# Performance work log

Measured on AMD Instinct MI355X. Metric: run time of the kernel, lower is better.

Reference implementation:

```python
import jax, jax.numpy as jnp
import numpy as np

N_U, N_I, D_IN_U, D_IN_I, D, D_QOL, B = 4096, 4096, 256, 256, 256, 4, 8192

def _w(key, shape, scale=0.05):
    return (jax.random.normal(key, shape) * scale).astype(jnp.float32)

def setup_inputs() -> dict:
    key = jax.random.key(0)
    ks = jax.random.split(key, 24)
    inp = {
        "x_u": jax.random.normal(ks[0], (N_U, D_IN_U), jnp.float32),
        "x_i": jax.random.normal(ks[1], (N_I, D_IN_I), jnp.float32),
        "social_adj": jax.random.randint(ks[2], (N_U, N_U), 0, 2, jnp.int32),
        "ui_adj": jax.random.randint(ks[3], (N_U, N_I), 0, 2, jnp.int32),
        "user_idx": jax.random.randint(ks[4], (B,), 0, N_U, jnp.int32),
        "item_idx": jax.random.randint(ks[5], (B,), 0, N_I, jnp.int32),
        "q_u": jax.random.normal(ks[6], (N_U, D_QOL), jnp.float32),
        # params (Linear stored as [in, out]; y = x @ W + b)
        "user_W": _w(ks[7], (D_IN_U, D)), "user_b": jnp.zeros((D,), jnp.float32),
        "item_W": _w(ks[8], (D_IN_I, D)), "item_b": jnp.zeros((D,), jnp.float32),
        "soc_W": _w(ks[9], (D, D)), "soc_a": _w(ks[10], (2 * D,)),
        "cnt_W": _w(ks[11], (D, D)), "cnt_a": _w(ks[12], (2 * D,)),
        "gate_W": _w(ks[13], (D_QOL, D)), "gate_b": jnp.zeros((D,), jnp.float32),
        "qproj_W": _w(ks[14], (D_QOL, D)), "qproj_b": jnp.zeros((D,), jnp.float32),
        "alpha_q": jnp.float32(0.3),
        "pred_W1": _w(ks[15], (2 * D, D)), "pred_b1": jnp.zeros((D,), jnp.float32),
        "pred_W2": _w(ks[16], (D, 1)), "pred_b2": jnp.zeros((1,), jnp.float32),
    }
    return inp

def _gat(Wh_src, Wh_dst, a, adj):
    """GAT additive attention: src rows attend over dst cols where adj!=0.
    Rows with no neighbors produce zero output (matches nan_to_num + zeroing)."""
    d = Wh_src.shape[-1]
    a1 = Wh_src @ a[:d]          # [N_src]
    a2 = Wh_dst @ a[d:]          # [N_dst]
    e = jax.nn.leaky_relu(a1[:, None] + a2[None, :], 0.2)  # [N_src, N_dst]
    mask = adj != 0
    neg_inf = jnp.float32(-jnp.inf)
    m = jnp.max(jnp.where(mask, e, neg_inf), axis=-1, keepdims=True)
    m = jnp.where(jnp.isfinite(m), m, 0.0)  # guard empty rows
    ex = jnp.where(mask, jnp.exp(e - m), 0.0)
    denom = jnp.sum(ex, axis=-1, keepdims=True)
    alpha = jnp.where(denom > 0, ex / jnp.where(denom > 0, denom, 1.0), 0.0)
    out = alpha @ Wh_dst
    return out, alpha

def reference(x_u, x_i, social_adj, ui_adj, user_idx, item_idx, q_u,
              user_W, user_b, item_W, item_b, soc_W, soc_a, cnt_W, cnt_a,
              gate_W, gate_b, qproj_W, qproj_b, alpha_q,
              pred_W1, pred_b1, pred_W2, pred_b2):
    h_u = x_u @ user_W + user_b               # [N_u, D]
    h_i = x_i @ item_W + item_b               # [N_i, D]
    # social attention (users over users)
    Wh = h_u @ soc_W
    soc_msg, alpha_s = _gat(Wh, Wh, soc_a, social_adj)
    # content attention (users over items)
    Wu = h_u @ cnt_W
    Wi = h_i @ cnt_W
    cnt_msg, alpha_c = _gat(Wu, Wi, cnt_a, ui_adj)
    h_u_out = jax.nn.elu(soc_msg + cnt_msg + h_u)
    # QoL gate
    gate = jax.nn.sigmoid(q_u @ gate_W + gate_b)
    qproj = q_u @ qproj_W + qproj_b
    h_u_out = h_u_out + alpha_q * gate * qproj
    # pair prediction (dropout inactive at eval)
    cat = jnp.concatenate([h_u_out[user_idx], h_i[item_idx]], axis=-1)  # [B, 2D]
    hid = jax.nn.relu(cat @ pred_W1 + pred_b1)
    r = (hid @ pred_W2 + pred_b2)[..., 0]
    r_hat = 1.0 + 4.0 * jax.nn.sigmoid(r)
    return r_hat, alpha_s, alpha_c
```

## Files before the change

kernel.cpp:

```cpp
#include <hip/hip_runtime.h>

typedef unsigned short u16;
typedef unsigned int u32;
typedef unsigned char u8;
typedef unsigned long long u64;
typedef float f32x4 __attribute__((ext_vector_type(4)));
typedef __bf16 bf16x8 __attribute__((ext_vector_type(8)));

#define NU 4096
#define DD 256
#define BB 8192

__device__ inline u16 f2b(float f) {
    u32 u = __builtin_bit_cast(u32, f);
    u32 r = (u + 0x7fffu + ((u >> 16) & 1u)) >> 16;
    return (u16)r;
}
__device__ inline float b2f(u16 v) { return __builtin_bit_cast(float, (u32)v << 16); }
__device__ inline float lrelu(float x) { return x > 0.f ? x : 0.2f * x; }
__device__ inline float decmax(u32 e) {
    return __builtin_bit_cast(float, (e >> 31) ? (e & 0x7fffffffu) : ~e);
}

#define BARRIER_LGKM() asm volatile("s_waitcnt lgkmcnt(0)\ns_barrier" ::: "memory")

__global__ __launch_bounds__(256) void k_pro(
    const float* __restrict__ x_u, const float* __restrict__ x_i,
    const float* __restrict__ user_W, const float* __restrict__ item_W, const float* __restrict__ pred_W1,
    const float* __restrict__ soc_W, const float* __restrict__ soc_a,
    const float* __restrict__ cnt_W, const float* __restrict__ cnt_a,
    const float* __restrict__ user_b, const float* __restrict__ item_b,
    u16* __restrict__ xu_b, u16* __restrict__ xi_b,
    u16* __restrict__ uWt, u16* __restrict__ iWt, u16* __restrict__ p1Wt,
    float* __restrict__ uvec,
    u16* __restrict__ WusT, u16* __restrict__ WicT,
    float* __restrict__ b_us, float* __restrict__ b_ic, u32* __restrict__ MhEnc) {
    __shared__ float t[64][65];
    __shared__ float sa[256];
    const int b = blockIdx.x;
    const int tid = threadIdx.x;

    if (b < 1024) {
        const float* in = (b < 512) ? x_u : x_i;
        u16* out = (b < 512) ? xu_b : xi_b;
        int i = (b & 511) * 256 + tid;
        const float4 v0 = *(const float4*)(in + (size_t)i * 8);
        const float4 v1 = *(const float4*)(in + (size_t)i * 8 + 4);
        u16 u[8] = {f2b(v0.x), f2b(v0.y), f2b(v0.z), f2b(v0.w),
                    f2b(v1.x), f2b(v1.y), f2b(v1.z), f2b(v1.w)};
        *(uint4*)(out + (size_t)i * 8) = *(uint4*)u;
    } else if (b < 1088) {
        int j = b - 1024;
        const float* in;
        u16* out;
        int R;
        if (j < 16) { in = user_W; out = uWt; R = 256; }
        else if (j < 32) { in = item_W; out = iWt; R = 256; j -= 16; }
        else { in = pred_W1; out = p1Wt; R = 512; j -= 32; }
        int rb = (j >> 2) * 64, cb = (j & 3) * 64;
        for (int k = 0; k < 16; ++k) {
            int idx = k * 256 + tid;
            int lr = idx >> 6, lc = idx & 63;
            t[lr][lc] = in[(size_t)(rb + lr) * 256 + cb + lc];
        }
        __syncthreads();
        for (int k = 0; k < 16; ++k) {
            int idx = k * 256 + tid;
            int lr = idx >> 6, lc = idx & 63;
            out[(size_t)(cb + lr) * R + rb + lc] = f2b(t[lc][lr]);
        }
    } else if (b < 1092) {
        int bb = b - 1088;
        if (bb == 0 && tid < 2) MhEnc[tid] = 0u;
        const float* W = (bb < 2) ? soc_W : cnt_W;
        const float* a = ((bb < 2) ? soc_a : cnt_a) + (bb & 1) * 256;
        int lane = tid & 63, wv = tid >> 6;
        sa[tid] = a[tid];
        __syncthreads();
        for (int rr = 0; rr < 64; ++rr) {
            int in = wv * 64 + rr;
            float4 w4 = *(const float4*)(W + (size_t)in * 256 + lane * 4);
            float acc = w4.x * sa[lane * 4] + w4.y * sa[lane * 4 + 1] + w4.z * sa[lane * 4 + 2] + w4.w * sa[lane * 4 + 3];
#pragma unroll
            for (int off = 32; off; off >>= 1) acc += __shfl_down(acc, off);
            if (lane == 0) uvec[bb * 256 + in] = acc;
        }
    } else {
        int j = b - 1092;
        int p = j >> 4;
        int tile = j & 15;
        const float* A = p ? item_W : user_W;
        const float* Bw = p ? cnt_W : soc_W;
        const float* bvec = p ? item_b : user_b;
        u16* outT = p ? WicT : WusT;
        float* outb = p ? b_ic : b_us;
        int m0 = (tile >> 2) * 64, n0 = (tile & 3) * 64;
        int m = m0 + (tid >> 4) * 4, n = n0 + (tid & 15) * 4;
        float acc[4][4];
#pragma unroll
        for (int i = 0; i < 4; ++i)
#pragma unroll
            for (int k = 0; k < 4; ++k) acc[i][k] = 0.f;
        for (int k0 = 0; k0 < 256; k0 += 4) {
            float aa[4][4], bb2[4][4];
#pragma unroll
            for (int i = 0; i < 4; ++i) {
                float4 v = *(const float4*)(A + (size_t)(m + i) * 256 + k0);
                aa[i][0] = v.x; aa[i][1] = v.y; aa[i][2] = v.z; aa[i][3] = v.w;
            }
#pragma unroll
            for (int k = 0; k < 4; ++k) {
                float4 v = *(const float4*)(Bw + (size_t)(k0 + k) * 256 + n);
                bb2[k][0] = v.x; bb2[k][1] = v.y; bb2[k][2] = v.z; bb2[k][3] = v.w;
            }
#pragma unroll
            for (int i = 0; i < 4; ++i)
#pragma unroll
                for (int k = 0; k < 4; ++k)
#pragma unroll
                    for (int jj = 0; jj < 4; ++jj) acc[i][jj] += aa[i][k] * bb2[k][jj];
        }
#pragma unroll
        for (int i = 0; i < 4; ++i)
#pragma unroll
            for (int jj = 0; jj < 4; ++jj) outT[(size_t)(n + jj) * 256 + m + i] = f2b(acc[i][jj]);
        if (tile >> 2 == 0 && tid < 64) {
            int nn = n0 + tid;
            float s = 0.f;
            for (int k = 0; k < 256; ++k) s += bvec[k] * Bw[(size_t)k * 256 + nn];
            outb[nn] = s;
        }
    }
}

__global__ __launch_bounds__(256) void k_gemm4(
    const u16* __restrict__ xu_b, const u16* __restrict__ xi_b,
    const u16* __restrict__ uWt, const u16* __restrict__ iWt,
    const u16* __restrict__ WusT, const u16* __restrict__ WicT,
    const float* __restrict__ user_b, const float* __restrict__ item_b,
    const float* __restrict__ b_us, const float* __restrict__ b_ic,
    float* __restrict__ h_u_f, float* __restrict__ h_i_f, u16* __restrict__ h_i_b,
    u16* __restrict__ WhT, u16* __restrict__ WiT) {
    const int z = blockIdx.z;
    const int M = 4096, N = 256, K = 256;
    const u16* A = (z == 0 || z == 2) ? xu_b : xi_b;
    const u16* Bt = (z == 0) ? uWt : (z == 1) ? iWt : (z == 2) ? WusT : WicT;
    const float* bias = (z == 0) ? user_b : (z == 1) ? item_b : (z == 2) ? b_us : b_ic;
    float* Cf = (z == 0) ? h_u_f : (z == 1) ? h_i_f : nullptr;
    u16* Cb = (z == 1) ? h_i_b : nullptr;
    u16* Cbt = (z == 2) ? WhT : (z == 3) ? WiT : nullptr;

    __shared__ u16 As[64 * 64];
    __shared__ u16 Bs[64 * 64];
    const int tid = threadIdx.x;
    const int lane = tid & 63, wv = tid >> 6;
    const int bm = blockIdx.x * 64, bn = blockIdx.y * 64;
    const int wm = (wv >> 1) * 32, wn = (wv & 1) * 32;
    f32x4 acc[2][2];
#pragma unroll
    for (int i = 0; i < 2; i++)
#pragma unroll
        for (int j = 0; j < 2; j++) acc[i][j] = f32x4{0.f, 0.f, 0.f, 0.f};

    char* Ab = (char*)As;
    char* Bb = (char*)Bs;
    const int r = tid >> 2;
    const int ib0 = (tid & 3) * 32;
    const int swz = (r & 7) << 4;

    for (int k0 = 0; k0 < K; k0 += 64) {
        const uint4* ga = (const uint4*)(A + (size_t)(bm + r) * K + k0 + (ib0 >> 1));
        const uint4* gb = (const uint4*)(Bt + (size_t)(bn + r) * K + k0 + (ib0 >> 1));
        uint4 va0 = ga[0], va1 = ga[1];
        uint4 vb0 = gb[0], vb1 = gb[1];
        __syncthreads();
        *(uint4*)(Ab + r * 128 + ((ib0) ^ swz)) = va0;
        *(uint4*)(Ab + r * 128 + ((ib0 + 16) ^ swz)) = va1;
        *(uint4*)(Bb + r * 128 + ((ib0) ^ swz)) = vb0;
        *(uint4*)(Bb + r * 128 + ((ib0 + 16) ^ swz)) = vb1;
        __syncthreads();
#pragma unroll
        for (int kh = 0; kh < 2; ++kh) {
            bf16x8 af[2], bfr[2];
#pragma unroll
            for (int mf = 0; mf < 2; ++mf) {
                int row = wm + mf * 16 + (lane & 15);
                int kb = kh * 64 + ((lane >> 4) << 4);
                af[mf] = *(const bf16x8*)(Ab + row * 128 + (kb ^ ((row & 7) << 4)));
            }
#pragma unroll
            for (int nf = 0; nf < 2; ++nf) {
                int row = wn + nf * 16 + (lane & 15);
                int kb = kh * 64 + ((lane >> 4) << 4);
                bfr[nf] = *(const bf16x8*)(Bb + row * 128 + (kb ^ ((row & 7) << 4)));
            }
#pragma unroll
            for (int mf = 0; mf < 2; ++mf)
#pragma unroll
                for (int nf = 0; nf < 2; ++nf)
                    acc[mf][nf] = __builtin_amdgcn_mfma_f32_16x16x32_bf16(af[mf], bfr[nf], acc[mf][nf], 0, 0, 0);
        }
    }
#pragma unroll
    for (int mf = 0; mf < 2; ++mf) {
#pragma unroll
        for (int nf = 0; nf < 2; ++nf) {
            int col = bn + wn + nf * 16 + (lane & 15);
            int row0 = bm + wm + mf * 16 + ((lane >> 4) << 2);
            float bv = bias[col];
            float v[4];
#pragma unroll
            for (int q = 0; q < 4; ++q) {
                float x = acc[mf][nf][q] + bv;
                v[q] = x;
                if (Cf) Cf[(size_t)(row0 + q) * N + col] = x;
                if (Cb) Cb[(size_t)(row0 + q) * N + col] = f2b(x);
            }
            if (Cbt) {
                uint2 p;
                p.x = (u32)f2b(v[0]) | ((u32)f2b(v[1]) << 16);
                p.y = (u32)f2b(v[2]) | ((u32)f2b(v[3]) << 16);
                *(uint2*)(Cbt + (size_t)col * M + row0) = p;
            }
        }
    }
}

__global__ __launch_bounds__(256) void k_gemv_a(const float* __restrict__ h_u, const float* __restrict__ h_i,
                                                const float* __restrict__ uvec, float* __restrict__ avec,
                                                u32* __restrict__ MhEnc) {
    int tid = threadIdx.x, lane = tid & 63, wv = tid >> 6;
    int ib = blockIdx.x * 64;
    const float* H = (wv == 3) ? h_i : h_u;
    const float* u = uvec + wv * 256;
    float4 u4 = *(const float4*)(u + lane * 4);
    float runm = -1e30f;
    for (int rr = 0; rr < 64; ++rr) {
        int row = ib + rr;
        float4 h4 = *(const float4*)(H + (size_t)row * 256 + lane * 4);
        float acc = h4.x * u4.x + h4.y * u4.y + h4.z * u4.z + h4.w * u4.w;
#pragma unroll
        for (int off = 32; off; off >>= 1) acc += __shfl_down(acc, off);
        if (lane == 0) {
            avec[wv * 4096 + row] = acc;
            runm = fmaxf(runm, acc);
        }
    }
    if (lane == 0 && (wv & 1)) {
        u32 b = __builtin_bit_cast(u32, runm);
        u32 e = (b >> 31) ? ~b : (b | 0x80000000u);
        atomicMax(&MhEnc[wv >> 1], e);
    }
}

__global__ __launch_bounds__(256) void k_scan(const int* __restrict__ adjS, const int* __restrict__ adjC,
                                              const float* __restrict__ avec, const u32* __restrict__ MhEnc,
                                              float* __restrict__ dpart, u8* __restrict__ bits) {
    int z = blockIdx.z;
    const int* adj = z ? adjC : adjS;
    const float* a1 = avec + z * 8192;
    const float* a2 = a1 + 4096;
    u8* bz = bits + (size_t)z * 2097152;
    float mhg = decmax(MhEnc[z]);
    int ib = blockIdx.x * 64, jb = blockIdx.y * 512;
    int lane = threadIdx.x & 63, wv = threadIdx.x >> 6;
    float4 A0 = *(const float4*)(a2 + jb + lane * 8);
    float4 A1 = *(const float4*)(a2 + jb + lane * 8 + 4);
    const int boff = blockIdx.y * 64 + (lane & 7) * 8 + (lane >> 3);
    for (int rr = 0; rr < 16; ++rr) {
        int row = ib + wv * 16 + rr;
        float a1r = a1[row];
        float mr = lrelu(a1r + mhg);
        const int4* p = (const int4*)(adj + (size_t)row * 4096 + jb + lane * 8);
        int4 v0 = p[0], v1 = p[1];
        u32 b = (u32)(v0.x != 0) | ((u32)(v0.y != 0) << 1) | ((u32)(v0.z != 0) << 2) | ((u32)(v0.w != 0) << 3) |
                ((u32)(v1.x != 0) << 4) | ((u32)(v1.y != 0) << 5) | ((u32)(v1.z != 0) << 6) | ((u32)(v1.w != 0) << 7);
        bz[(size_t)row * 512 + boff] = (u8)b;
        float acc = 0.f;
        acc += v0.x ? __expf(lrelu(a1r + A0.x) - mr) : 0.f;
        acc += v0.y ? __expf(lrelu(a1r + A0.y) - mr) : 0.f;
        acc += v0.z ? __expf(lrelu(a1r + A0.z) - mr) : 0.f;
        acc += v0.w ? __expf(lrelu(a1r + A0.w) - mr) : 0.f;
        acc += v1.x ? __expf(lrelu(a1r + A1.x) - mr) : 0.f;
        acc += v1.y ? __expf(lrelu(a1r + A1.y) - mr) : 0.f;
        acc += v1.z ? __expf(lrelu(a1r + A1.z) - mr) : 0.f;
        acc += v1.w ? __expf(lrelu(a1r + A1.w) - mr) : 0.f;
#pragma unroll
        for (int off = 32; off; off >>= 1) acc += __shfl_down(acc, off);
        if (lane == 0) dpart[((size_t)z * 8 + blockIdx.y) * 4096 + row] = acc;
    }
}

__global__ __launch_bounds__(512, 4) void k_flash(const u8* __restrict__ bits,
                                                  const float* __restrict__ avec, const u32* __restrict__ MhEnc,
                                                  const float* __restrict__ dpart,
                                                  const u16* __restrict__ WhT, const u16* __restrict__ WiT,
                                                  float* __restrict__ out, u16* __restrict__ msgpart) {
    const int z = blockIdx.z;
    const int ib = blockIdx.x * 64;
    const int jb = blockIdx.y * 512;
    const int tid = threadIdx.x, lane = tid & 63, wv = tid >> 6;
    const u8* bz = bits + (size_t)z * 2097152;
    const float* a1 = avec + z * 8192;
    const float* a2 = a1 + 4096;
    const u16* Pt = z ? WiT : WhT;
    float* alpha = out + 8192 + (size_t)z * 16777216;

    __shared__ float a2s[512];
    __shared__ u16 Atile[2 * 64 * 64];
    __shared__ float s_a1[64], s_mr[64], s_inv[64];
    char* Ab = (char*)Atile;

    a2s[tid] = a2[jb + tid];
    if (tid < 64) {
        float a = a1[ib + tid];
        float mhg = decmax(MhEnc[z]);
        s_a1[tid] = a;
        s_mr[tid] = lrelu(a + mhg);
        float d = 0.f;
#pragma unroll
        for (int s = 0; s < 8; ++s) d += dpart[((size_t)(z * 8 + s)) * 4096 + ib + tid];
        s_inv[tid] = d > 0.f ? 1.f / d : 0.f;
    }
    __syncthreads();

    const int row = wv * 8 + (lane >> 3);
    const int cg = lane & 7;
    const int gr = ib + row;
    const u64 b64 = *(const u64*)(bz + (size_t)gr * 512 + (jb >> 9) * 64 + cg * 8);
    const float a1r = s_a1[row], mr = s_mr[row], ivr = s_inv[row];
    const int wswz = (row & 7) << 4;

    const u16* ptb0 = Pt + (size_t)(wv * 32 + (lane & 15)) * 4096 + jb + ((lane >> 4) << 3);
    const u16* ptb1 = ptb0 + (size_t)16 * 4096;

    f32x4 acc[4][2];
#pragma unroll
    for (int i = 0; i < 4; i++)
#pragma unroll
        for (int j = 0; j < 2; j++) acc[i][j] = f32x4{0.f, 0.f, 0.f, 0.f};

    float al[8];
    auto compute_al = [&](int js, int buf) {
        const float4 a2a = *(const float4*)(a2s + js * 64 + cg * 8);
        const float4 a2b = *(const float4*)(a2s + js * 64 + cg * 8 + 4);
        u32 byte = (u32)(b64 >> (js * 8)) & 0xffu;
        float av[8] = {a2a.x, a2a.y, a2a.z, a2a.w, a2b.x, a2b.y, a2b.z, a2b.w};
#pragma unroll
        for (int k = 0; k < 8; ++k) {
            float e = lrelu(a1r + av[k]) - mr;
            al[k] = ((byte >> k) & 1) ? __expf(e) * ivr : 0.f;
        }
        u16 pk[8];
#pragma unroll
        for (int k = 0; k < 8; ++k) pk[k] = f2b(al[k]);
        *(uint4*)(Ab + buf * 8192 + row * 128 + ((cg * 16) ^ wswz)) = *(uint4*)pk;
    };

    compute_al(0, 0);
    BARRIER_LGKM();

    bf16x8 bcur[2][2], bnxt[2][2];
#pragma unroll
    for (int kh = 0; kh < 2; ++kh) {
        bcur[kh][0] = *(const bf16x8*)(ptb0 + kh * 32);
        bcur[kh][1] = *(const bf16x8*)(ptb1 + kh * 32);
    }

    for (int js = 0; js < 8; ++js) {
        const int buf = js & 1;
        {
            float4 sA = {al[0], al[1], al[2], al[3]};
            float4 sB = {al[4], al[5], al[6], al[7]};
            float* ap = alpha + (size_t)gr * 4096 + jb + js * 64 + cg * 8;
            *(float4*)ap = sA;
            *(float4*)(ap + 4) = sB;
        }
        if (js < 7) {
#pragma unroll
            for (int kh = 0; kh < 2; ++kh) {
                bnxt[kh][0] = *(const bf16x8*)(ptb0 + (js + 1) * 64 + kh * 32);
                bnxt[kh][1] = *(const bf16x8*)(ptb1 + (js + 1) * 64 + kh * 32);
            }
        }
#pragma unroll
        for (int kh = 0; kh < 2; ++kh) {
#pragma unroll
            for (int mf = 0; mf < 4; ++mf) {
                int ra = mf * 16 + (lane & 15);
                int kb = kh * 64 + ((lane >> 4) << 4);
                bf16x8 af = *(const bf16x8*)(Ab + buf * 8192 + ra * 128 + (kb ^ ((ra & 7) << 4)));
#pragma unroll
                for (int nf = 0; nf < 2; ++nf)
                    acc[mf][nf] = __builtin_amdgcn_mfma_f32_16x16x32_bf16(af, bcur[kh][nf], acc[mf][nf], 0, 0, 0);
            }
        }
        if (js < 7) compute_al(js + 1, buf ^ 1);
        BARRIER_LGKM();
        if (js < 7) {
#pragma unroll
            for (int kh = 0; kh < 2; ++kh) {
                bcur[kh][0] = bnxt[kh][0];
                bcur[kh][1] = bnxt[kh][1];
            }
        }
    }

    u16* mp = msgpart + ((size_t)(z * 8 + blockIdx.y) * 4096 + ib) * 256;
#pragma unroll
    for (int mf = 0; mf < 4; ++mf) {
        int r0 = mf * 16 + ((lane >> 4) << 2);
#pragma unroll
        for (int nf = 0; nf < 2; ++nf) {
            int col = wv * 32 + nf * 16 + (lane & 15);
#pragma unroll
            for (int q = 0; q < 4; ++q) mp[(size_t)(r0 + q) * 256 + col] = f2b(acc[mf][nf][q]);
        }
    }
}

__global__ __launch_bounds__(256) void k_post(const u16* __restrict__ msgpart, const float* __restrict__ h_u,
                                              const float* __restrict__ q_u,
                                              const float* __restrict__ gate_W, const float* __restrict__ gate_b,
                                              const float* __restrict__ qproj_W, const float* __restrict__ qproj_b,
                                              const float* __restrict__ alpha_q, u16* __restrict__ huo_b) {
    int i = blockIdx.x;
    int n = threadIdx.x;
    float s = 0.f;
#pragma unroll
    for (int p = 0; p < 16; ++p) s += b2f(msgpart[((size_t)p * 4096 + i) * 256 + n]);
    float v = s + h_u[(size_t)i * 256 + n];
    v = v > 0.f ? v : expm1f(v);
    float q0 = q_u[i * 4 + 0], q1 = q_u[i * 4 + 1], q2 = q_u[i * 4 + 2], q3 = q_u[i * 4 + 3];
    float g = q0 * gate_W[n] + q1 * gate_W[256 + n] + q2 * gate_W[512 + n] + q3 * gate_W[768 + n] + gate_b[n];
    g = 1.f / (1.f + __expf(-g));
    float qp = q0 * qproj_W[n] + q1 * qproj_W[256 + n] + q2 * qproj_W[512 + n] + q3 * qproj_W[768 + n] + qproj_b[n];
    float o = v + alpha_q[0] * g * qp;
    huo_b[(size_t)i * 256 + n] = f2b(o);
}

__global__ __launch_bounds__(512) void k_pred(const u16* __restrict__ huo_b, const u16* __restrict__ h_i_b,
                                              const int* __restrict__ uidx, const int* __restrict__ iidx,
                                              const u16* __restrict__ Bt, const float* __restrict__ b1,
                                              const float* __restrict__ W2, const float* __restrict__ b2,
                                              float* __restrict__ out) {
    __shared__ u16 As[64 * 512];
    __shared__ float redL[512];
    const int tid = threadIdx.x, lane = tid & 63, wv = tid >> 6;
    const int bm = blockIdx.x * 64;
    char* Ab = (char*)As;

    {
        const int r = tid >> 3;
        const int uix = uidx[bm + r], iix = iidx[bm + r];
        const int sswz = (r & 7) << 4;
#pragma unroll
        for (int c = 0; c < 8; ++c) {
            int e = c * 64 + (tid & 7) * 8;
            const u16* src = (e < 256) ? (huo_b + (size_t)uix * 256 + e) : (h_i_b + (size_t)iix * 256 + (e - 256));
            uint4 v = *(const uint4*)src;
            *(uint4*)(Ab + r * 1024 + ((e * 2) ^ sswz)) = v;
        }
    }
    __syncthreads();

    const int n0 = wv * 32;
    f32x4 acc[4][2];
#pragma unroll
    for (int i = 0; i < 4; i++)
#pragma unroll
        for (int j = 0; j < 2; j++) acc[i][j] = f32x4{0.f, 0.f, 0.f, 0.f};

    for (int ks = 0; ks < 16; ++ks) {
        bf16x8 bfr[2];
#pragma unroll
        for (int nf = 0; nf < 2; ++nf)
            bfr[nf] = *(const bf16x8*)(Bt + (size_t)(n0 + nf * 16 + (lane & 15)) * 512 + ks * 32 + ((lane >> 4) << 3));
#pragma unroll
        for (int mf = 0; mf < 4; ++mf) {
            int ra = mf * 16 + (lane & 15);
            bf16x8 af = *(const bf16x8*)(Ab + ra * 1024 + ((ks * 64 + ((lane >> 4) << 4)) ^ ((ra & 7) << 4)));
#pragma unroll
            for (int nf = 0; nf < 2; ++nf)
                acc[mf][nf] = __builtin_amdgcn_mfma_f32_16x16x32_bf16(af, bfr[nf], acc[mf][nf], 0, 0, 0);
        }
    }

    float b1v[2], w2v[2];
#pragma unroll
    for (int nf = 0; nf < 2; ++nf) {
        int col = n0 + nf * 16 + (lane & 15);
        b1v[nf] = b1[col];
        w2v[nf] = W2[col];
    }
#pragma unroll
    for (int mf = 0; mf < 4; ++mf) {
#pragma unroll
        for (int q = 0; q < 4; ++q) {
            float val = 0.f;
#pragma unroll
            for (int nf = 0; nf < 2; ++nf) val += fmaxf(acc[mf][nf][q] + b1v[nf], 0.f) * w2v[nf];
#pragma unroll
            for (int off = 1; off < 16; off <<= 1) val += __shfl_xor(val, off);
            if ((lane & 15) == 0) redL[wv * 64 + mf * 16 + ((lane >> 4) << 2) + q] = val;
        }
    }
    __syncthreads();
    if (tid < 64) {
        float r = b2[0];
#pragma unroll
        for (int w = 0; w < 8; ++w) r += redL[w * 64 + tid];
        out[bm + tid] = 1.f + 4.f / (1.f + __expf(-r));
    }
}

extern "C" void kernel_launch(void* const* d_in, const int* in_sizes, int n_in,
                              void* d_out, int out_size, void* d_ws, size_t ws_size,
                              hipStream_t stream) {
    const float* x_u = (const float*)d_in[0];
    const float* x_i = (const float*)d_in[1];
    const int* adjS = (const int*)d_in[2];
    const int* adjC = (const int*)d_in[3];
    const int* uidx = (const int*)d_in[4];
    const int* iidx = (const int*)d_in[5];
    const float* q_u = (const float*)d_in[6];
    const float* user_W = (const float*)d_in[7];
    const float* user_b = (const float*)d_in[8];
    const float* item_W = (const float*)d_in[9];
    const float* item_b = (const float*)d_in[10];
    const float* soc_W = (const float*)d_in[11];
    const float* soc_a = (const float*)d_in[12];
    const float* cnt_W = (const float*)d_in[13];
    const float* cnt_a = (const float*)d_in[14];
    const float* gate_W = (const float*)d_in[15];
    const float* gate_b = (const float*)d_in[16];
    const float* qproj_W = (const float*)d_in[17];
    const float* qproj_b = (const float*)d_in[18];
    const float* alpha_q = (const float*)d_in[19];
    const float* pred_W1 = (const float*)d_in[20];
    const float* pred_b1 = (const float*)d_in[21];
    const float* pred_W2 = (const float*)d_in[22];
    const float* pred_b2 = (const float*)d_in[23];
    float* out = (float*)d_out;

    char* w = (char*)d_ws;
    size_t off = 0;
    auto alloc = [&](size_t bytes) -> void* {
        void* p = w + off;
        off = (off + bytes + 255) & ~(size_t)255;
        return p;
    };
    u16* xu_b = (u16*)alloc((size_t)NU * DD * 2);
    u16* xi_b = (u16*)alloc((size_t)NU * DD * 2);
    u16* uWt = (u16*)alloc(256 * 256 * 2);
    u16* iWt = (u16*)alloc(256 * 256 * 2);
    u16* p1Wt = (u16*)alloc(512 * 256 * 2);
    u16* WusT = (u16*)alloc(256 * 256 * 2);
    u16* WicT = (u16*)alloc(256 * 256 * 2);
    float* b_us = (float*)alloc(256 * 4);
    float* b_ic = (float*)alloc(256 * 4);
    float* uvec = (float*)alloc(4 * 256 * 4);
    float* h_u_f = (float*)alloc((size_t)NU * DD * 4);
    float* h_i_f = (float*)alloc((size_t)NU * DD * 4);
    u16* h_i_b = (u16*)alloc((size_t)NU * DD * 2);
    u16* WhT = (u16*)alloc((size_t)NU * DD * 2);
    u16* WiT = (u16*)alloc((size_t)NU * DD * 2);
    float* avec = (float*)alloc(4 * 4096 * 4);
    u32* MhEnc = (u32*)alloc(2 * 4);
    float* dpart = (float*)alloc((size_t)2 * 8 * 4096 * 4);
    u8* bits = (u8*)alloc((size_t)2 * 2097152);
    u16* msgpart = (u16*)alloc((size_t)16 * 4096 * 256 * 2);
    u16* huo_b = (u16*)alloc((size_t)NU * DD * 2);
    (void)in_sizes; (void)n_in; (void)out_size; (void)ws_size;

    k_pro<<<1124, 256, 0, stream>>>(x_u, x_i, user_W, item_W, pred_W1, soc_W, soc_a, cnt_W, cnt_a,
                                    user_b, item_b, xu_b, xi_b, uWt, iWt, p1Wt, uvec, WusT, WicT,
                                    b_us, b_ic, MhEnc);
    k_gemm4<<<dim3(64, 4, 4), 256, 0, stream>>>(xu_b, xi_b, uWt, iWt, WusT, WicT, user_b, item_b, b_us, b_ic,
                                                h_u_f, h_i_f, h_i_b, WhT, WiT);
    k_gemv_a<<<64, 256, 0, stream>>>(h_u_f, h_i_f, uvec, avec, MhEnc);
    k_scan<<<dim3(64, 8, 2), 256, 0, stream>>>(adjS, adjC, avec, MhEnc, dpart, bits);
    k_flash<<<dim3(64, 8, 2), 512, 0, stream>>>(bits, avec, MhEnc, dpart, WhT, WiT, out, msgpart);
    k_post<<<4096, 256, 0, stream>>>(msgpart, h_u_f, q_u, gate_W, gate_b, qproj_W, qproj_b, alpha_q, huo_b);
    k_pred<<<128, 512, 0, stream>>>(huo_b, h_i_b, uidx, iidx, p1Wt, pred_b1, pred_W2, pred_b2, out);
}
```

Measured before the change: 189.6 us.

## Widen flash attention column tile to 1024 and halve message partials

The flash kernel now covers 1024 columns per block in two 512-column passes. Each pass builds the full 64x512 bf16 alpha tile in shared memory before running the MFMA loop, replacing the per-64-column double-buffered interleave. The scan kernel's mask byte layout is changed to be lane-contiguous so flash reads bytes per row directly, and the number of message partials drops from 16 to 8, which cuts msgpart writes and the reads in k_post. In exchange there is less overlap between alpha computation and MFMA, a larger shared footprint (64KB tile) that lowers occupancy, and half as many blocks.

```diff
diff --git a/kernel.cpp b/kernel.cpp
--- a/kernel.cpp
+++ b/kernel.cpp
@@ -266,7 +266,7 @@
     int lane = threadIdx.x & 63, wv = threadIdx.x >> 6;
     float4 A0 = *(const float4*)(a2 + jb + lane * 8);
     float4 A1 = *(const float4*)(a2 + jb + lane * 8 + 4);
-    const int boff = blockIdx.y * 64 + (lane & 7) * 8 + (lane >> 3);
+    const int boff = (jb >> 3) + lane;
     for (int rr = 0; rr < 16; ++rr) {
         int row = ib + wv * 16 + rr;
         float a1r = a1[row];
@@ -298,7 +298,7 @@
                                                   float* __restrict__ out, u16* __restrict__ msgpart) {
     const int z = blockIdx.z;
     const int ib = blockIdx.x * 64;
-    const int jb = blockIdx.y * 512;
+    const int jb0 = blockIdx.y * 1024;
     const int tid = threadIdx.x, lane = tid & 63, wv = tid >> 6;
     const u8* bz = bits + (size_t)z * 2097152;
     const float* a1 = avec + z * 8192;
@@ -306,107 +306,89 @@
     const u16* Pt = z ? WiT : WhT;
     float* alpha = out + 8192 + (size_t)z * 16777216;
 
-    __shared__ float a2s[512];
-    __shared__ u16 Atile[2 * 64 * 64];
+    __shared__ float a2s[1024];
     __shared__ float s_a1[64], s_mr[64], s_inv[64];
+    __shared__ u16 Atile[64 * 512];
     char* Ab = (char*)Atile;
 
-    a2s[tid] = a2[jb + tid];
-    if (tid < 64) {
-        float a = a1[ib + tid];
-        float mhg = decmax(MhEnc[z]);
-        s_a1[tid] = a;
-        s_mr[tid] = lrelu(a + mhg);
-        float d = 0.f;
-#pragma unroll
-        for (int s = 0; s < 8; ++s) d += dpart[((size_t)(z * 8 + s)) * 4096 + ib + tid];
-        s_inv[tid] = d > 0.f ? 1.f / d : 0.f;
+    {
+        float2 v = *(const float2*)(a2 + jb0 + tid * 2);
+        *(float2*)(a2s + tid * 2) = v;
+        if (tid < 64) {
+            float a = a1[ib + tid];
+            float mhg = decmax(MhEnc[z]);
+            s_a1[tid] = a;
+            s_mr[tid] = lrelu(a + mhg);
+            float d = 0.f;
+#pragma unroll
+            for (int s = 0; s < 8; ++s) d += dpart[((size_t)(z * 8 + s)) * 4096 + ib + tid];
+            s_inv[tid] = d > 0.f ? 1.f / d : 0.f;
+        }
     }
     __syncthreads();
 
-    const int row = wv * 8 + (lane >> 3);
-    const int cg = lane & 7;
-    const int gr = ib + row;
-    const u64 b64 = *(const u64*)(bz + (size_t)gr * 512 + (jb >> 9) * 64 + cg * 8);
-    const float a1r = s_a1[row], mr = s_mr[row], ivr = s_inv[row];
-    const int wswz = (row & 7) << 4;
-
-    const u16* ptb0 = Pt + (size_t)(wv * 32 + (lane & 15)) * 4096 + jb + ((lane >> 4) << 3);
-    const u16* ptb1 = ptb0 + (size_t)16 * 4096;
-
     f32x4 acc[4][2];
 #pragma unroll
     for (int i = 0; i < 4; i++)
 #pragma unroll
         for (int j = 0; j < 2; j++) acc[i][j] = f32x4{0.f, 0.f, 0.f, 0.f};
 
-    float al[8];
-    auto compute_al = [&](int js, int buf) {
-        const float4 a2a = *(const float4*)(a2s + js * 64 + cg * 8);
-        const float4 a2b = *(const float4*)(a2s + js * 64 + cg * 8 + 4);
-        u32 byte = (u32)(b64 >> (js * 8)) & 0xffu;
-        float av[8] = {a2a.x, a2a.y, a2a.z, a2a.w, a2b.x, a2b.y, a2b.z, a2b.w};
-#pragma unroll
-        for (int k = 0; k < 8; ++k) {
-            float e = lrelu(a1r + av[k]) - mr;
-            al[k] = ((byte >> k) & 1) ? __expf(e) * ivr : 0.f;
-        }
-        u16 pk[8];
-#pragma unroll
-        for (int k = 0; k < 8; ++k) pk[k] = f2b(al[k]);
-        *(uint4*)(Ab + buf * 8192 + row * 128 + ((cg * 16) ^ wswz)) = *(uint4*)pk;
-    };
-
-    compute_al(0, 0);
-    BARRIER_LGKM();
-
-    bf16x8 bcur[2][2], bnxt[2][2];
-#pragma unroll
-    for (int kh = 0; kh < 2; ++kh) {
-        bcur[kh][0] = *(const bf16x8*)(ptb0 + kh * 32);
-        bcur[kh][1] = *(const bf16x8*)(ptb1 + kh * 32);
-    }
-
-    for (int js = 0; js < 8; ++js) {
-        const int buf = js & 1;
-        {
-            float4 sA = {al[0], al[1], al[2], al[3]};
-            float4 sB = {al[4], al[5], al[6], al[7]};
-            float* ap = alpha + (size_t)gr * 4096 + jb + js * 64 + cg * 8;
-            *(float4*)ap = sA;
-            *(float4*)(ap + 4) = sB;
-        }
-        if (js < 7) {
-#pragma unroll
-            for (int kh = 0; kh < 2; ++kh) {
-                bnxt[kh][0] = *(const bf16x8*)(ptb0 + (js + 1) * 64 + kh * 32);
-                bnxt[kh][1] = *(const bf16x8*)(ptb1 + (js + 1) * 64 + kh * 32);
-            }
-        }
-#pragma unroll
-        for (int kh = 0; kh < 2; ++kh) {
+    const u16* ptb = Pt + (size_t)(wv * 32 + (lane & 15)) * 4096 + jb0 + ((lane >> 4) << 3);
+
+    for (int sub = 0; sub < 2; ++sub) {
+        const int jb = jb0 + sub * 512;
+        const int bcol = (jb >> 3) + lane;
+        u8 bvv[8];
+#pragma unroll
+        for (int rs = 0; rs < 8; ++rs)
+            bvv[rs] = bz[(size_t)(ib + rs * 8 + wv) * 512 + bcol];
+        const float4 a2a = *(const float4*)(a2s + sub * 512 + lane * 8);
+        const float4 a2b = *(const float4*)(a2s + sub * 512 + lane * 8 + 4);
+        const float av[8] = {a2a.x, a2a.y, a2a.z, a2a.w, a2b.x, a2b.y, a2b.z, a2b.w};
+#pragma unroll
+        for (int rs = 0; rs < 8; ++rs) {
+            const int r = rs * 8 + wv;
+            const float a1r = s_a1[r], mr = s_mr[r], ivr = s_inv[r];
+            const u32 byte = bvv[rs];
+            float al[8];
+#pragma unroll
+            for (int k = 0; k < 8; ++k) {
+                float e = lrelu(a1r + av[k]) - mr;
+                al[k] = ((byte >> k) & 1) ? __expf(e) * ivr : 0.f;
+            }
+            float* ap = alpha + (size_t)(ib + r) * 4096 + jb + lane * 8;
+            *(float4*)ap = float4{al[0], al[1], al[2], al[3]};
+            *(float4*)(ap + 4) = float4{al[4], al[5], al[6], al[7]};
+            u16 pk[8];
+#pragma unroll
+            for (int k = 0; k < 8; ++k) pk[k] = f2b(al[k]);
+            *(uint4*)(Ab + r * 1024 + ((lane * 16) ^ ((r & 7) << 4))) = *(uint4*)pk;
+        }
+        BARRIER_LGKM();
+
+        const u16* pts = ptb + sub * 512;
+        bf16x8 bcur0 = *(const bf16x8*)(pts);
+        bf16x8 bcur1 = *(const bf16x8*)(pts + (size_t)16 * 4096);
+        for (int ks = 0; ks < 16; ++ks) {
+            bf16x8 bnxt0, bnxt1;
+            if (ks < 15) {
+                bnxt0 = *(const bf16x8*)(pts + (ks + 1) * 32);
+                bnxt1 = *(const bf16x8*)(pts + (size_t)16 * 4096 + (ks + 1) * 32);
+            }
 #pragma unroll
             for (int mf = 0; mf < 4; ++mf) {
                 int ra = mf * 16 + (lane & 15);
-                int kb = kh * 64 + ((lane >> 4) << 4);
-                bf16x8 af = *(const bf16x8*)(Ab + buf * 8192 + ra * 128 + (kb ^ ((ra & 7) << 4)));
-#pragma unroll
-                for (int nf = 0; nf < 2; ++nf)
-                    acc[mf][nf] = __builtin_amdgcn_mfma_f32_16x16x32_bf16(af, bcur[kh][nf], acc[mf][nf], 0, 0, 0);
-            }
-        }
-        if (js < 7) compute_al(js + 1, buf ^ 1);
+                bf16x8 af = *(const bf16x8*)(Ab + ra * 1024 + ((ks * 64 + ((lane >> 4) << 4)) ^ ((ra & 7) << 4)));
+                acc[mf][0] = __builtin_amdgcn_mfma_f32_16x16x32_bf16(af, bcur0, acc[mf][0], 0, 0, 0);
+                acc[mf][1] = __builtin_amdgcn_mfma_f32_16x16x32_bf16(af, bcur1, acc[mf][1], 0, 0, 0);
+            }
+            bcur0 = bnxt0;
+            bcur1 = bnxt1;
+        }
         BARRIER_LGKM();
-        if (js < 7) {
-#pragma unroll
-            for (int kh = 0; kh < 2; ++kh) {
-                bcur[kh][0] = bnxt[kh][0];
-                bcur[kh][1] = bnxt[kh][1];
-            }
-        }
-    }
-
-    u16* mp = msgpart + ((size_t)(z * 8 + blockIdx.y) * 4096 + ib) * 256;
+    }
+
+    u16* mp = msgpart + ((size_t)(z * 4 + blockIdx.y) * 4096 + ib) * 256;
 #pragma unroll
     for (int mf = 0; mf < 4; ++mf) {
         int r0 = mf * 16 + ((lane >> 4) << 2);
@@ -428,7 +410,7 @@
     int n = threadIdx.x;
     float s = 0.f;
 #pragma unroll
-    for (int p = 0; p < 16; ++p) s += b2f(msgpart[((size_t)p * 4096 + i) * 256 + n]);
+    for (int p = 0; p < 8; ++p) s += b2f(msgpart[((size_t)p * 4096 + i) * 256 + n]);
     float v = s + h_u[(size_t)i * 256 + n];
     v = v > 0.f ? v : expm1f(v);
     float q0 = q_u[i * 4 + 0], q1 = q_u[i * 4 + 1], q2 = q_u[i * 4 + 2], q3 = q_u[i * 4 + 3];
@@ -569,7 +551,7 @@
     u32* MhEnc = (u32*)alloc(2 * 4);
     float* dpart = (float*)alloc((size_t)2 * 8 * 4096 * 4);
     u8* bits = (u8*)alloc((size_t)2 * 2097152);
-    u16* msgpart = (u16*)alloc((size_t)16 * 4096 * 256 * 2);
+    u16* msgpart = (u16*)alloc((size_t)8 * 4096 * 256 * 2);
     u16* huo_b = (u16*)alloc((size_t)NU * DD * 2);
     (void)in_sizes; (void)n_in; (void)out_size; (void)ws_size;
 
@@ -580,7 +562,7 @@
                                                 h_u_f, h_i_f, h_i_b, WhT, WiT);
     k_gemv_a<<<64, 256, 0, stream>>>(h_u_f, h_i_f, uvec, avec, MhEnc);
     k_scan<<<dim3(64, 8, 2), 256, 0, stream>>>(adjS, adjC, avec, MhEnc, dpart, bits);
-    k_flash<<<dim3(64, 8, 2), 512, 0, stream>>>(bits, avec, MhEnc, dpart, WhT, WiT, out, msgpart);
+    k_flash<<<dim3(64, 4, 2), 512, 0, stream>>>(bits, avec, MhEnc, dpart, WhT, WiT, out, msgpart);
     k_post<<<4096, 256, 0, stream>>>(msgpart, h_u_f, q_u, gate_W, gate_b, qproj_W, qproj_b, alpha_q, huo_b);
     k_pred<<<128, 512, 0, stream>>>(huo_b, h_i_b, uidx, iidx, p1Wt, pred_b1, pred_W2, pred_b2, out);
 }
```

New measurement: 194.3 us. 2.5% more time.
